# Optimization experiments

Measured on AMD Instinct MI355X. Metric: run time of the kernel, lower is better.

The kernel has to match this reference:

```python
import jax, jax.numpy as jnp
import numpy as np


def setup_inputs() -> dict:
    key = jax.random.key(0)
    k1, k2, k3 = jax.random.split(key, 3)
    B, N, D = 4, 4096, 1024
    x = jax.random.normal(k1, (B, N, D), dtype=jnp.float32)
    # torch nn.Linear default init ~ U(-1/sqrt(D), 1/sqrt(D)); scale normals similarly
    scale = 1.0 / np.sqrt(D)
    Wq = jax.random.normal(k2, (D, D), dtype=jnp.float32) * scale
    Wk = jax.random.normal(k3, (D, D), dtype=jnp.float32) * scale
    return {"x": x, "Wq": Wq, "Wk": Wk}


def reference(x, Wq, Wk):
    # torch Linear: y = x @ W.T (weight shape [out, in])
    D = x.shape[-1]
    q = jnp.einsum('bnd,ed->bne', x, Wq)  # [B,N,D]
    k = jnp.einsum('bnd,ed->bne', x, Wk)  # [B,N,D]
    scores = jnp.einsum('bqd,bkd->bqk', q, k) / jnp.sqrt(jnp.float32(D))
    attn = jax.nn.softmax(scores, axis=-1)  # [B,N,N]
    return jnp.einsum('bqk,bkd->bqd', attn, x)
```

## Files before the change

### kernel.cpp

```cpp
#include <hip/hip_runtime.h>
#include <stdint.h>
#include <math.h>

typedef __attribute__((ext_vector_type(8))) short short8;
typedef __attribute__((ext_vector_type(4))) float fx4;
typedef unsigned int u32;

#define MFMA16(a, b, c) __builtin_amdgcn_mfma_f32_16x16x32_bf16(a, b, c, 0, 0, 0)
#define SCL 0.04508422002777948f

#define CFENCE asm volatile("" ::: "memory")

__device__ __forceinline__ unsigned short f2bfu(float f) {
  unsigned u = __builtin_bit_cast(unsigned, f);
  u += 0x7fffu + ((u >> 16) & 1u);
  return (unsigned short)(u >> 16);
}

__device__ __forceinline__ float fast_exp2(float x) {
  float r;
  asm("v_exp_f32 %0, %1" : "=v"(r) : "v"(x));
  return r;
}

__device__ __forceinline__ void gl_lds16(const void* g, void* l) {
  __builtin_amdgcn_global_load_lds(
      (const __attribute__((address_space(1))) u32*)g,
      (__attribute__((address_space(3))) u32*)l, 16, 0, 0);
}

__device__ __forceinline__ void barx() {
  CFENCE;
  __builtin_amdgcn_s_barrier();
  CFENCE;
}

__global__ __launch_bounds__(256) void prep_kernel(const float* __restrict__ x,
                                                   unsigned short* __restrict__ xT,
                                                   unsigned short* __restrict__ xbf) {
  __shared__ float tile[64 * 65];
  const int b = blockIdx.z, n0 = blockIdx.x * 64, d0 = blockIdx.y * 64;
  const int tid = threadIdx.x;
  const float* xb = x + ((size_t)b * 4096 + n0) * 1024 + d0;
#pragma unroll
  for (int i = 0; i < 4; i++) {
    int idx = tid + 256 * i;
    int r = idx >> 4, c4 = (idx & 15) * 4;
    const float4 v = *(const float4*)(xb + (size_t)r * 1024 + c4);
    float* tp = &tile[r * 65 + c4];
    tp[0] = v.x; tp[1] = v.y; tp[2] = v.z; tp[3] = v.w;
    uint2 pkt;
    pkt.x = (u32)f2bfu(v.x) | ((u32)f2bfu(v.y) << 16);
    pkt.y = (u32)f2bfu(v.z) | ((u32)f2bfu(v.w) << 16);
    *(uint2*)(xbf + ((size_t)b * 4096 + n0 + r) * 1024 + d0 + c4) = pkt;
  }
  __syncthreads();
  unsigned short* xo = xT + ((size_t)b * 1024 + d0) * 4096 + n0;
#pragma unroll
  for (int i = 0; i < 4; i++) {
    int idx = tid + 256 * i;
    int dr = idx >> 4, n4 = (idx & 15) * 4;
    unsigned short h0 = f2bfu(tile[(n4 + 0) * 65 + dr]);
    unsigned short h1 = f2bfu(tile[(n4 + 1) * 65 + dr]);
    unsigned short h2 = f2bfu(tile[(n4 + 2) * 65 + dr]);
    unsigned short h3 = f2bfu(tile[(n4 + 3) * 65 + dr]);
    uint2 pkt;
    pkt.x = (u32)h0 | ((u32)h1 << 16);
    pkt.y = (u32)h2 | ((u32)h3 << 16);
    *(uint2*)(xo + (size_t)dr * 4096 + n4) = pkt;
  }
}

__global__ __launch_bounds__(256) void wconv_kernel(const float* __restrict__ Wq,
                                                    const float* __restrict__ Wk,
                                                    unsigned short* __restrict__ Wqb,
                                                    unsigned short* __restrict__ Wkb) {
  int gid = blockIdx.x * 256 + threadIdx.x;
  const float* s = (gid < 262144) ? Wq : Wk;
  unsigned short* d = (gid < 262144) ? Wqb : Wkb;
  int off = (gid & 262143) * 4;
  const float4 v = *(const float4*)(s + off);
  uint2 pkt;
  pkt.x = (u32)f2bfu(v.x) | ((u32)f2bfu(v.y) << 16);
  pkt.y = (u32)f2bfu(v.z) | ((u32)f2bfu(v.w) << 16);
  *(uint2*)(d + off) = pkt;
}


template <int ONES, int NT, int LDA, int LDB>
__device__ __forceinline__ void core128(const unsigned short* __restrict__ Ab,
                                        const unsigned short* __restrict__ Bb,
                                        short* lds, fx4 (&acc)[4][4], fx4 (&accl)[4]) {
  constexpr int BUFB = 49152;
  const int tid = threadIdx.x;
  const int wave = tid >> 6, lane = tid & 63;
  const int wm = wave >> 1, wn = wave & 1;
  const int quad = lane >> 4, l16 = lane & 15;
  char* lp = (char*)lds;

  const int sr0 = tid >> 3, so0 = (tid & 7) ^ (sr0 & 7);
  const int ga0 = sr0 * LDA + so0 * 8;
  const int ga1 = ga0 + 64 * LDA;
  const int gb0 = sr0 * LDB + so0 * 8;
  const int ld0 = tid * 16;

  const int cst0 = (quad ^ (l16 & 7)) * 16;
  const int cst1 = ((4 + quad) ^ (l16 & 7)) * 16;
  const int arb = (wm >> 1) * 16384 + (wm & 1) * 8192 + l16 * 128;
  const int brb = 32768 + wn * 8192 + l16 * 128;

  short8 ones;
#pragma unroll
  for (int i = 0; i < 8; i++) ones[i] = (short)0x3F80;
#pragma unroll
  for (int i = 0; i < 4; i++) {
    accl[i] = (fx4)0.f;
#pragma unroll
    for (int j = 0; j < 4; j++) acc[i][j] = (fx4)0.f;
  }

#define PV_STGA(halfb, rowadd, bufb, kte)                                          \
  do {                                                                             \
    gl_lds16(Ab + (size_t)(rowadd) * LDA + (kte) + ga0, lp + (bufb) + (halfb) + ld0); \
    gl_lds16(Ab + (size_t)(rowadd) * LDA + (kte) + ga1,                            \
             lp + (bufb) + (halfb) + ld0 + 8192);                                  \
  } while (0)
#define PV_STGB(halfb, rowadd, bufb, kte) \
  gl_lds16(Bb + (size_t)(rowadd) * LDB + (kte) + gb0, lp + (bufb) + 32768 + (halfb) + ld0)

  PV_STGB(0, 0, 0, 0);
  PV_STGA(0, 0, 0, 0);
  PV_STGA(16384, 128, 0, 0);
  PV_STGB(8192, 64, 0, 0);
  PV_STGB(0, 0, BUFB, 64);
  PV_STGA(0, 0, BUFB, 64);
  asm volatile("s_waitcnt vmcnt(3)" ::: "memory");
  barx();

  short8 af[4], bf0[4], bf1[4];
  for (int t = 0; t < NT; ++t) {
    const int cbo = (t & 1) * BUFB, nbo = cbo ^ BUFB;
    const int kt1 = ((t + 1) & (NT - 1)) * 64;
    const int kt2 = ((t + 2) & (NT - 1)) * 64;
#pragma unroll
    for (int mt = 0; mt < 2; mt++) {
      af[2 * mt] = *(const short8*)(lp + cbo + arb + mt * 2048 + cst0);
      af[2 * mt + 1] = *(const short8*)(lp + cbo + arb + mt * 2048 + cst1);
    }
#pragma unroll
    for (int nt = 0; nt < 2; nt++) {
      bf0[2 * nt] = *(const short8*)(lp + cbo + brb + nt * 2048 + cst0);
      bf0[2 * nt + 1] = *(const short8*)(lp + cbo + brb + nt * 2048 + cst1);
    }
    PV_STGA(16384, 128, nbo, kt1);
    barx();
    __builtin_amdgcn_s_setprio(1);
#pragma unroll
    for (int mt = 0; mt < 2; mt++) {
#pragma unroll
      for (int nt = 0; nt < 2; nt++) {
        acc[mt][nt] = MFMA16(af[2 * mt], bf0[2 * nt], acc[mt][nt]);
        acc[mt][nt] = MFMA16(af[2 * mt + 1], bf0[2 * nt + 1], acc[mt][nt]);
      }
      if (ONES) {
        accl[mt] = MFMA16(af[2 * mt], ones, accl[mt]);
        accl[mt] = MFMA16(af[2 * mt + 1], ones, accl[mt]);
      }
    }
    __builtin_amdgcn_s_setprio(0);
    barx();
#pragma unroll
    for (int nt = 0; nt < 2; nt++) {
      bf1[2 * nt] = *(const short8*)(lp + cbo + brb + (nt + 2) * 2048 + cst0);
      bf1[2 * nt + 1] = *(const short8*)(lp + cbo + brb + (nt + 2) * 2048 + cst1);
    }
    PV_STGB(8192, 64, nbo, kt1);
    barx();
    __builtin_amdgcn_s_setprio(1);
#pragma unroll
    for (int mt = 0; mt < 2; mt++)
#pragma unroll
      for (int nt = 0; nt < 2; nt++) {
        acc[mt][nt + 2] = MFMA16(af[2 * mt], bf1[2 * nt], acc[mt][nt + 2]);
        acc[mt][nt + 2] = MFMA16(af[2 * mt + 1], bf1[2 * nt + 1], acc[mt][nt + 2]);
      }
    __builtin_amdgcn_s_setprio(0);
    barx();
#pragma unroll
    for (int mt = 0; mt < 2; mt++) {
      af[2 * mt] = *(const short8*)(lp + cbo + arb + (mt + 2) * 2048 + cst0);
      af[2 * mt + 1] = *(const short8*)(lp + cbo + arb + (mt + 2) * 2048 + cst1);
    }
    PV_STGB(0, 0, cbo, kt2);
    barx();
    __builtin_amdgcn_s_setprio(1);
#pragma unroll
    for (int mt = 0; mt < 2; mt++) {
#pragma unroll
      for (int nt = 0; nt < 2; nt++) {
        acc[mt + 2][nt + 2] = MFMA16(af[2 * mt], bf1[2 * nt], acc[mt + 2][nt + 2]);
        acc[mt + 2][nt + 2] = MFMA16(af[2 * mt + 1], bf1[2 * nt + 1], acc[mt + 2][nt + 2]);
      }
      if (ONES) {
        accl[mt + 2] = MFMA16(af[2 * mt], ones, accl[mt + 2]);
        accl[mt + 2] = MFMA16(af[2 * mt + 1], ones, accl[mt + 2]);
      }
    }
    __builtin_amdgcn_s_setprio(0);
    barx();
    PV_STGA(0, 0, cbo, kt2);
    asm volatile("s_waitcnt vmcnt(3)" ::: "memory");
    barx();
    __builtin_amdgcn_s_setprio(1);
#pragma unroll
    for (int mt = 0; mt < 2; mt++)
#pragma unroll
      for (int nt = 0; nt < 2; nt++) {
        acc[mt + 2][nt] = MFMA16(af[2 * mt], bf0[2 * nt], acc[mt + 2][nt]);
        acc[mt + 2][nt] = MFMA16(af[2 * mt + 1], bf0[2 * nt + 1], acc[mt + 2][nt]);
      }
    __builtin_amdgcn_s_setprio(0);
    barx();
  }
#undef PV_STGA
#undef PV_STGB
}

__global__ __launch_bounds__(512) void proj_kernel(
    const unsigned short* __restrict__ xbf, const unsigned short* __restrict__ Wqb,
    const unsigned short* __restrict__ Wkb, unsigned short* __restrict__ Qo,
    unsigned short* __restrict__ Ko) {
  __shared__ __attribute__((aligned(16))) short lds[49152];
  const unsigned short* Wb = blockIdx.z ? Wkb : Wqb;
  unsigned short* O = blockIdx.z ? Ko : Qo;
  const int m0 = blockIdx.x * 256, e0 = blockIdx.y * 128;
  fx4 acc[4][4], accl[4];
  core128<0, 16, 1024, 1024>(xbf + (size_t)m0 * 1024, Wb + (size_t)e0 * 1024, lds, acc, accl);
  const int wave = threadIdx.x >> 6, lane = threadIdx.x & 63;
  const int wm = wave >> 1, wn = wave & 1;
  const int quad = lane >> 4, l16 = lane & 15;
#pragma unroll
  for (int mt = 0; mt < 4; mt++) {
    const int row = m0 + wm * 64 + mt * 16 + quad * 4;
#pragma unroll
    for (int nt = 0; nt < 4; nt++) {
      const int col = e0 + wn * 64 + nt * 16 + l16;
      unsigned short* op = O + (size_t)row * 1024 + col;
#pragma unroll
      for (int i = 0; i < 4; i++) op[(size_t)i * 1024] = f2bfu(acc[mt][nt][i]);
    }
  }
}

__global__ __launch_bounds__(512) void pv_kernel(
    const unsigned short* __restrict__ P, const unsigned short* __restrict__ xT,
    unsigned short* __restrict__ Ost, int bbase) {
  __shared__ __attribute__((aligned(16))) short lds[49152];
  const int bz = blockIdx.z, b = bbase + bz;
  const int m0 = blockIdx.x * 256, e0 = blockIdx.y * 128;
  const unsigned short* Ab = P + (size_t)bz * 4096 * 4096 + (size_t)m0 * 4096;
  const unsigned short* Bb = xT + (size_t)b * 1024 * 4096 + (size_t)e0 * 4096;
  fx4 acc[4][4], accl[4];
  core128<1, 64, 4096, 4096>(Ab, Bb, lds, acc, accl);
  unsigned short* O = Ost + (size_t)b * 4096 * 1024;
  const int wave = threadIdx.x >> 6, lane = threadIdx.x & 63;
  const int wm = wave >> 1, wn = wave & 1;
  const int quad = lane >> 4, l16 = lane & 15;
#pragma unroll
  for (int mt = 0; mt < 4; mt++) {
    const int row = m0 + wm * 64 + mt * 16 + quad * 4;
    const fx4 li = accl[mt];
    fx4 r;
#pragma unroll
    for (int i = 0; i < 4; i++) r[i] = __builtin_amdgcn_rcpf(li[i]);
#pragma unroll
    for (int nt = 0; nt < 4; nt++) {
      const int col = e0 + wn * 64 + nt * 16 + l16;
      unsigned short* op = O + (size_t)row * 1024 + col;
#pragma unroll
      for (int i = 0; i < 4; i++) op[(size_t)i * 1024] = f2bfu(acc[mt][nt][i] * r[i]);
    }
  }
}

__global__ __launch_bounds__(512) void qk_kernel(
    const unsigned short* __restrict__ Qb, const unsigned short* __restrict__ Kb,
    unsigned short* __restrict__ Pp, int bbase) {
  constexpr int NT = 16;
  __shared__ __attribute__((aligned(16))) short lds[65536];
  const int bz = blockIdx.z, b = bbase + bz;
  const unsigned short* A = Qb + (size_t)b * 4096 * 1024;
  const unsigned short* Bm = Kb + (size_t)b * 4096 * 1024;
  unsigned short* Pb = Pp + (size_t)bz * 4096 * 4096;
  const int m0 = blockIdx.x * 256, n0 = blockIdx.y * 256;
  const int tid = threadIdx.x;
  const int wave = tid >> 6, lane = tid & 63;
  const int wm = wave >> 2, wn = wave & 3;
  const int quad = lane >> 4, l16 = lane & 15;
  char* lp = (char*)lds;

  const unsigned short* Ab = A + (size_t)m0 * 1024;
  const unsigned short* Bb = Bm + (size_t)n0 * 1024;
  const int sr0 = tid >> 3, so0 = (tid & 7) ^ (sr0 & 7);
  const int ga0 = sr0 * 1024 + so0 * 8;
  const int ga1 = ga0 + 64 * 1024;
  const int ld0 = tid * 16;

  const int cst0 = (quad ^ (l16 & 7)) * 16;
  const int cst1 = ((4 + quad) ^ (l16 & 7)) * 16;
  const int arb = wm * 16384 + l16 * 128;
  const int brb = 32768 + (wn >> 1) * 16384 + (wn & 1) * 8192 + l16 * 128;

  fx4 acc[8][4];
#pragma unroll
  for (int i = 0; i < 8; i++)
#pragma unroll
    for (int j = 0; j < 4; j++) acc[i][j] = (fx4)0.f;

#define QK_STG(OPb, halfb, rowadd, bufb, kte)                                       \
  do {                                                                              \
    gl_lds16(OPb + (size_t)(rowadd) * 1024 + (kte) + ga0, lp + (bufb) + (halfb) + ld0); \
    gl_lds16(OPb + (size_t)(rowadd) * 1024 + (kte) + ga1,                           \
             lp + (bufb) + (halfb) + ld0 + 8192);                                   \
  } while (0)

  QK_STG(Bb, 32768, 0, 0, 0);
  QK_STG(Ab, 0, 0, 0, 0);
  QK_STG(Ab, 16384, 128, 0, 0);
  QK_STG(Bb, 49152, 128, 0, 0);
  QK_STG(Bb, 32768, 0, 65536, 64);
  QK_STG(Ab, 0, 0, 65536, 64);
  asm volatile("s_waitcnt vmcnt(4)" ::: "memory");
  barx();

  short8 af[8], bf0[4], bf1[4];
  for (int t = 0; t < NT; ++t) {
    const int cbo = (t & 1) * 65536, nbo = cbo ^ 65536;
    const int kt1 = ((t + 1) & (NT - 1)) * 64;
    const int kt2 = ((t + 2) & (NT - 1)) * 64;
#pragma unroll
    for (int mt = 0; mt < 4; mt++) {
      af[2 * mt] = *(const short8*)(lp + cbo + arb + mt * 2048 + cst0);
      af[2 * mt + 1] = *(const short8*)(lp + cbo + arb + mt * 2048 + cst1);
    }
#pragma unroll
    for (int nt = 0; nt < 2; nt++) {
      bf0[2 * nt] = *(const short8*)(lp + cbo + brb + nt * 2048 + cst0);
      bf0[2 * nt + 1] = *(const short8*)(lp + cbo + brb + nt * 2048 + cst1);
    }
    QK_STG(Ab, 16384, 128, nbo, kt1);
    barx();
    __builtin_amdgcn_s_setprio(1);
#pragma unroll
    for (int mt = 0; mt < 4; mt++)
#pragma unroll
      for (int nt = 0; nt < 2; nt++) {
        acc[mt][nt] = MFMA16(af[2 * mt], bf0[2 * nt], acc[mt][nt]);
        acc[mt][nt] = MFMA16(af[2 * mt + 1], bf0[2 * nt + 1], acc[mt][nt]);
      }
    __builtin_amdgcn_s_setprio(0);
    barx();
#pragma unroll
    for (int nt = 0; nt < 2; nt++) {
      bf1[2 * nt] = *(const short8*)(lp + cbo + brb + (nt + 2) * 2048 + cst0);
      bf1[2 * nt + 1] = *(const short8*)(lp + cbo + brb + (nt + 2) * 2048 + cst1);
    }
    QK_STG(Bb, 49152, 128, nbo, kt1);
    barx();
    __builtin_amdgcn_s_setprio(1);
#pragma unroll
    for (int mt = 0; mt < 4; mt++)
#pragma unroll
      for (int nt = 0; nt < 2; nt++) {
        acc[mt][nt + 2] = MFMA16(af[2 * mt], bf1[2 * nt], acc[mt][nt + 2]);
        acc[mt][nt + 2] = MFMA16(af[2 * mt + 1], bf1[2 * nt + 1], acc[mt][nt + 2]);
      }
    __builtin_amdgcn_s_setprio(0);
    barx();
#pragma unroll
    for (int mt = 0; mt < 4; mt++) {
      af[2 * mt] = *(const short8*)(lp + cbo + arb + (mt + 4) * 2048 + cst0);
      af[2 * mt + 1] = *(const short8*)(lp + cbo + arb + (mt + 4) * 2048 + cst1);
    }
    QK_STG(Bb, 32768, 0, cbo, kt2);
    barx();
    __builtin_amdgcn_s_setprio(1);
#pragma unroll
    for (int mt = 0; mt < 4; mt++)
#pragma unroll
      for (int nt = 0; nt < 2; nt++) {
        acc[mt + 4][nt + 2] = MFMA16(af[2 * mt], bf1[2 * nt], acc[mt + 4][nt + 2]);
        acc[mt + 4][nt + 2] = MFMA16(af[2 * mt + 1], bf1[2 * nt + 1], acc[mt + 4][nt + 2]);
      }
    __builtin_amdgcn_s_setprio(0);
    barx();
    QK_STG(Ab, 0, 0, cbo, kt2);
    asm volatile("s_waitcnt vmcnt(4)" ::: "memory");
    barx();
    __builtin_amdgcn_s_setprio(1);
#pragma unroll
    for (int mt = 0; mt < 4; mt++)
#pragma unroll
      for (int nt = 0; nt < 2; nt++) {
        acc[mt + 4][nt] = MFMA16(af[2 * mt], bf0[2 * nt], acc[mt + 4][nt]);
        acc[mt + 4][nt] = MFMA16(af[2 * mt + 1], bf0[2 * nt + 1], acc[mt + 4][nt]);
      }
    __builtin_amdgcn_s_setprio(0);
    barx();
  }
#undef QK_STG
#pragma unroll
  for (int mt = 0; mt < 8; mt++) {
    const int row = m0 + wm * 128 + mt * 16 + quad * 4;
#pragma unroll
    for (int nt = 0; nt < 4; nt++) {
      const int col = n0 + wn * 64 + nt * 16 + l16;
      unsigned short* pp = Pb + (size_t)row * 4096 + col;
#pragma unroll
      for (int i = 0; i < 4; i++)
        pp[(size_t)i * 4096] = f2bfu(fast_exp2(acc[mt][nt][i] * SCL));
    }
  }
}

__global__ __launch_bounds__(256) void fin_kernel(const uint4* __restrict__ Ost,
                                                  float4* __restrict__ out) {
  size_t t = (size_t)blockIdx.x * 256 + threadIdx.x;
  const uint4 v = Ost[t];
  float4 o0, o1;
  o0.x = __builtin_bit_cast(float, v.x << 16);
  o0.y = __builtin_bit_cast(float, v.x & 0xffff0000u);
  o0.z = __builtin_bit_cast(float, v.y << 16);
  o0.w = __builtin_bit_cast(float, v.y & 0xffff0000u);
  o1.x = __builtin_bit_cast(float, v.z << 16);
  o1.y = __builtin_bit_cast(float, v.z & 0xffff0000u);
  o1.z = __builtin_bit_cast(float, v.w << 16);
  o1.w = __builtin_bit_cast(float, v.w & 0xffff0000u);
  out[t * 2] = o0;
  out[t * 2 + 1] = o1;
}

extern "C" void kernel_launch(void* const* d_in, const int* in_sizes, int n_in,
                              void* d_out, int out_size, void* d_ws, size_t ws_size,
                              hipStream_t stream) {
  const float* x = (const float*)d_in[0];
  const float* Wq = (const float*)d_in[1];
  const float* Wk = (const float*)d_in[2];
  char* ws = (char*)d_ws;
  unsigned short* xT = (unsigned short*)ws;
  unsigned short* Qb = (unsigned short*)(ws + (size_t)33554432);
  unsigned short* Kb = (unsigned short*)(ws + (size_t)67108864);
  unsigned short* Ost = Qb;
  unsigned short* xbf = (unsigned short*)d_out;
  unsigned short* Wqb = (unsigned short*)((char*)d_out + (size_t)33554432);
  unsigned short* Wkb = (unsigned short*)((char*)d_out + (size_t)35651584);
  unsigned short* Pp = (unsigned short*)d_out;

  hipLaunchKernelGGL(prep_kernel, dim3(64, 16, 4), dim3(256), 0, stream, x, xT, xbf);
  hipLaunchKernelGGL(wconv_kernel, dim3(2048), dim3(256), 0, stream, Wq, Wk, Wqb, Wkb);
  hipLaunchKernelGGL(proj_kernel, dim3(64, 8, 2), dim3(512), 0, stream, xbf, Wqb, Wkb, Qb, Kb);
  hipLaunchKernelGGL(qk_kernel, dim3(16, 16, 2), dim3(512), 0, stream, Qb, Kb, Pp, 0);
  hipLaunchKernelGGL(pv_kernel, dim3(16, 8, 2), dim3(512), 0, stream, Pp, xT, Ost, 0);
  hipLaunchKernelGGL(qk_kernel, dim3(16, 16, 2), dim3(512), 0, stream, Qb, Kb, Pp, 2);
  hipLaunchKernelGGL(pv_kernel, dim3(16, 8, 2), dim3(512), 0, stream, Pp, xT, Ost, 2);
  hipLaunchKernelGGL(fin_kernel, dim3(8192), dim3(256), 0, stream,
                     (const uint4*)Ost, (float4*)d_out);
}
```

Measured before the change: 497.1 us.

## Share 256x256 GEMM core for projection and swizzle block order in QK/PV

```diff
diff --git a/kernel.cpp b/kernel.cpp
--- a/kernel.cpp
+++ b/kernel.cpp
@@ -86,6 +86,123 @@
   *(uint2*)(d + off) = pkt;
 }
 
+__device__ __forceinline__ void core256(const unsigned short* __restrict__ Ab,
+                                        const unsigned short* __restrict__ Bb,
+                                        char* lp, fx4 (&acc)[8][4]) {
+  constexpr int NT = 16;
+  const int tid = threadIdx.x;
+  const int wave = tid >> 6, lane = tid & 63;
+  const int wm = wave >> 2, wn = wave & 3;
+  const int quad = lane >> 4, l16 = lane & 15;
+
+  const int sr0 = tid >> 3, so0 = (tid & 7) ^ (sr0 & 7);
+  const int ga0 = sr0 * 1024 + so0 * 8;
+  const int ga1 = ga0 + 64 * 1024;
+  const int ld0 = tid * 16;
+
+  const int cst0 = (quad ^ (l16 & 7)) * 16;
+  const int cst1 = ((4 + quad) ^ (l16 & 7)) * 16;
+  const int arb = wm * 16384 + l16 * 128;
+  const int brb = 32768 + (wn >> 1) * 16384 + (wn & 1) * 8192 + l16 * 128;
+
+#pragma unroll
+  for (int i = 0; i < 8; i++)
+#pragma unroll
+    for (int j = 0; j < 4; j++) acc[i][j] = (fx4)0.f;
+
+#define C_STG(OPb, halfb, rowadd, bufb, kte)                                        \
+  do {                                                                              \
+    gl_lds16(OPb + (size_t)(rowadd) * 1024 + (kte) + ga0, lp + (bufb) + (halfb) + ld0); \
+    gl_lds16(OPb + (size_t)(rowadd) * 1024 + (kte) + ga1,                           \
+             lp + (bufb) + (halfb) + ld0 + 8192);                                   \
+  } while (0)
+
+  C_STG(Bb, 32768, 0, 0, 0);
+  C_STG(Ab, 0, 0, 0, 0);
+  C_STG(Ab, 16384, 128, 0, 0);
+  C_STG(Bb, 49152, 128, 0, 0);
+  C_STG(Bb, 32768, 0, 65536, 64);
+  C_STG(Ab, 0, 0, 65536, 64);
+  asm volatile("s_waitcnt vmcnt(4)" ::: "memory");
+  barx();
+
+  short8 af[8], bf0[4], bf1[4];
+  for (int t = 0; t < NT; ++t) {
+    const int cbo = (t & 1) * 65536, nbo = cbo ^ 65536;
+    const int kt1 = ((t + 1) & (NT - 1)) * 64;
+    const int kt2 = ((t + 2) & (NT - 1)) * 64;
+#pragma unroll
+    for (int mt = 0; mt < 4; mt++) {
+      af[2 * mt] = *(const short8*)(lp + cbo + arb + mt * 2048 + cst0);
+      af[2 * mt + 1] = *(const short8*)(lp + cbo + arb + mt * 2048 + cst1);
+    }
+#pragma unroll
+    for (int nt = 0; nt < 2; nt++) {
+      bf0[2 * nt] = *(const short8*)(lp + cbo + brb + nt * 2048 + cst0);
+      bf0[2 * nt + 1] = *(const short8*)(lp + cbo + brb + nt * 2048 + cst1);
+    }
+    C_STG(Ab, 16384, 128, nbo, kt1);
+    barx();
+    __builtin_amdgcn_s_setprio(1);
+#pragma unroll
+    for (int mt = 0; mt < 4; mt++)
+#pragma unroll
+      for (int nt = 0; nt < 2; nt++) {
+        acc[mt][nt] = MFMA16(af[2 * mt], bf0[2 * nt], acc[mt][nt]);
+        acc[mt][nt] = MFMA16(af[2 * mt + 1], bf0[2 * nt + 1], acc[mt][nt]);
+      }
+    __builtin_amdgcn_s_setprio(0);
+    barx();
+#pragma unroll
+    for (int nt = 0; nt < 2; nt++) {
+      bf1[2 * nt] = *(const short8*)(lp + cbo + brb + (nt + 2) * 2048 + cst0);
+      bf1[2 * nt + 1] = *(const short8*)(lp + cbo + brb + (nt + 2) * 2048 + cst1);
+    }
+    C_STG(Bb, 49152, 128, nbo, kt1);
+    barx();
+    __builtin_amdgcn_s_setprio(1);
+#pragma unroll
+    for (int mt = 0; mt < 4; mt++)
+#pragma unroll
+      for (int nt = 0; nt < 2; nt++) {
+        acc[mt][nt + 2] = MFMA16(af[2 * mt], bf1[2 * nt], acc[mt][nt + 2]);
+        acc[mt][nt + 2] = MFMA16(af[2 * mt + 1], bf1[2 * nt + 1], acc[mt][nt + 2]);
+      }
+    __builtin_amdgcn_s_setprio(0);
+    barx();
+#pragma unroll
+    for (int mt = 0; mt < 4; mt++) {
+      af[2 * mt] = *(const short8*)(lp + cbo + arb + (mt + 4) * 2048 + cst0);
+      af[2 * mt + 1] = *(const short8*)(lp + cbo + arb + (mt + 4) * 2048 + cst1);
+    }
+    C_STG(Bb, 32768, 0, cbo, kt2);
+    barx();
+    __builtin_amdgcn_s_setprio(1);
+#pragma unroll
+    for (int mt = 0; mt < 4; mt++)
+#pragma unroll
+      for (int nt = 0; nt < 2; nt++) {
+        acc[mt + 4][nt + 2] = MFMA16(af[2 * mt], bf1[2 * nt], acc[mt + 4][nt + 2]);
+        acc[mt + 4][nt + 2] = MFMA16(af[2 * mt + 1], bf1[2 * nt + 1], acc[mt + 4][nt + 2]);
+      }
+    __builtin_amdgcn_s_setprio(0);
+    barx();
+    C_STG(Ab, 0, 0, cbo, kt2);
+    asm volatile("s_waitcnt vmcnt(4)" ::: "memory");
+    barx();
+    __builtin_amdgcn_s_setprio(1);
+#pragma unroll
+    for (int mt = 0; mt < 4; mt++)
+#pragma unroll
+      for (int nt = 0; nt < 2; nt++) {
+        acc[mt + 4][nt] = MFMA16(af[2 * mt], bf0[2 * nt], acc[mt + 4][nt]);
+        acc[mt + 4][nt] = MFMA16(af[2 * mt + 1], bf0[2 * nt + 1], acc[mt + 4][nt]);
+      }
+    __builtin_amdgcn_s_setprio(0);
+    barx();
+  }
+#undef C_STG
+}
 
 template <int ONES, int NT, int LDA, int LDB>
 __device__ __forceinline__ void core128(const unsigned short* __restrict__ Ab,
@@ -230,24 +347,54 @@
     const unsigned short* __restrict__ xbf, const unsigned short* __restrict__ Wqb,
     const unsigned short* __restrict__ Wkb, unsigned short* __restrict__ Qo,
     unsigned short* __restrict__ Ko) {
-  __shared__ __attribute__((aligned(16))) short lds[49152];
+  __shared__ __attribute__((aligned(16))) short lds[65536];
   const unsigned short* Wb = blockIdx.z ? Wkb : Wqb;
   unsigned short* O = blockIdx.z ? Ko : Qo;
-  const int m0 = blockIdx.x * 256, e0 = blockIdx.y * 128;
-  fx4 acc[4][4], accl[4];
-  core128<0, 16, 1024, 1024>(xbf + (size_t)m0 * 1024, Wb + (size_t)e0 * 1024, lds, acc, accl);
+  const int m0 = blockIdx.x * 256, e0 = blockIdx.y * 256;
+  fx4 acc[8][4];
+  core256(xbf + (size_t)m0 * 1024, Wb + (size_t)e0 * 1024, (char*)lds, acc);
   const int wave = threadIdx.x >> 6, lane = threadIdx.x & 63;
-  const int wm = wave >> 1, wn = wave & 1;
+  const int wm = wave >> 2, wn = wave & 3;
   const int quad = lane >> 4, l16 = lane & 15;
 #pragma unroll
-  for (int mt = 0; mt < 4; mt++) {
-    const int row = m0 + wm * 64 + mt * 16 + quad * 4;
+  for (int mt = 0; mt < 8; mt++) {
+    const int row = m0 + wm * 128 + mt * 16 + quad * 4;
 #pragma unroll
     for (int nt = 0; nt < 4; nt++) {
       const int col = e0 + wn * 64 + nt * 16 + l16;
       unsigned short* op = O + (size_t)row * 1024 + col;
 #pragma unroll
       for (int i = 0; i < 4; i++) op[(size_t)i * 1024] = f2bfu(acc[mt][nt][i]);
+    }
+  }
+}
+
+__global__ __launch_bounds__(512) void qk_kernel(
+    const unsigned short* __restrict__ Qb, const unsigned short* __restrict__ Kb,
+    unsigned short* __restrict__ Pp, int bbase) {
+  __shared__ __attribute__((aligned(16))) short lds[65536];
+  const int fid = blockIdx.x + 16 * blockIdx.y + 256 * blockIdx.z;
+  const int swz = (fid & 7) * 64 + (fid >> 3);
+  const int bx = swz & 15, by = (swz >> 4) & 15, bz = swz >> 8;
+  const int b = bbase + bz;
+  unsigned short* Pb = Pp + (size_t)bz * 4096 * 4096;
+  const int m0 = bx * 256, n0 = by * 256;
+  fx4 acc[8][4];
+  core256(Qb + (size_t)b * 4096 * 1024 + (size_t)m0 * 1024,
+          Kb + (size_t)b * 4096 * 1024 + (size_t)n0 * 1024, (char*)lds, acc);
+  const int wave = threadIdx.x >> 6, lane = threadIdx.x & 63;
+  const int wm = wave >> 2, wn = wave & 3;
+  const int quad = lane >> 4, l16 = lane & 15;
+#pragma unroll
+  for (int mt = 0; mt < 8; mt++) {
+    const int row = m0 + wm * 128 + mt * 16 + quad * 4;
+#pragma unroll
+    for (int nt = 0; nt < 4; nt++) {
+      const int col = n0 + wn * 64 + nt * 16 + l16;
+      unsigned short* pp = Pb + (size_t)row * 4096 + col;
+#pragma unroll
+      for (int i = 0; i < 4; i++)
+        pp[(size_t)i * 4096] = f2bfu(fast_exp2(acc[mt][nt][i] * SCL));
     }
   }
 }
@@ -256,8 +403,11 @@
     const unsigned short* __restrict__ P, const unsigned short* __restrict__ xT,
     unsigned short* __restrict__ Ost, int bbase) {
   __shared__ __attribute__((aligned(16))) short lds[49152];
-  const int bz = blockIdx.z, b = bbase + bz;
-  const int m0 = blockIdx.x * 256, e0 = blockIdx.y * 128;
+  const int fid = blockIdx.x + 16 * blockIdx.y + 128 * blockIdx.z;
+  const int swz = (fid & 7) * 32 + (fid >> 3);
+  const int bx = swz & 15, by = (swz >> 4) & 7, bz = swz >> 7;
+  const int b = bbase + bz;
+  const int m0 = bx * 256, e0 = by * 128;
   const unsigned short* Ab = P + (size_t)bz * 4096 * 4096 + (size_t)m0 * 4096;
   const unsigned short* Bb = xT + (size_t)b * 1024 * 4096 + (size_t)e0 * 4096;
   fx4 acc[4][4], accl[4];
@@ -279,146 +429,6 @@
       unsigned short* op = O + (size_t)row * 1024 + col;
 #pragma unroll
       for (int i = 0; i < 4; i++) op[(size_t)i * 1024] = f2bfu(acc[mt][nt][i] * r[i]);
-    }
-  }
-}
-
-__global__ __launch_bounds__(512) void qk_kernel(
-    const unsigned short* __restrict__ Qb, const unsigned short* __restrict__ Kb,
-    unsigned short* __restrict__ Pp, int bbase) {
-  constexpr int NT = 16;
-  __shared__ __attribute__((aligned(16))) short lds[65536];
-  const int bz = blockIdx.z, b = bbase + bz;
-  const unsigned short* A = Qb + (size_t)b * 4096 * 1024;
-  const unsigned short* Bm = Kb + (size_t)b * 4096 * 1024;
-  unsigned short* Pb = Pp + (size_t)bz * 4096 * 4096;
-  const int m0 = blockIdx.x * 256, n0 = blockIdx.y * 256;
-  const int tid = threadIdx.x;
-  const int wave = tid >> 6, lane = tid & 63;
-  const int wm = wave >> 2, wn = wave & 3;
-  const int quad = lane >> 4, l16 = lane & 15;
-  char* lp = (char*)lds;
-
-  const unsigned short* Ab = A + (size_t)m0 * 1024;
-  const unsigned short* Bb = Bm + (size_t)n0 * 1024;
-  const int sr0 = tid >> 3, so0 = (tid & 7) ^ (sr0 & 7);
-  const int ga0 = sr0 * 1024 + so0 * 8;
-  const int ga1 = ga0 + 64 * 1024;
-  const int ld0 = tid * 16;
-
-  const int cst0 = (quad ^ (l16 & 7)) * 16;
-  const int cst1 = ((4 + quad) ^ (l16 & 7)) * 16;
-  const int arb = wm * 16384 + l16 * 128;
-  const int brb = 32768 + (wn >> 1) * 16384 + (wn & 1) * 8192 + l16 * 128;
-
-  fx4 acc[8][4];
-#pragma unroll
-  for (int i = 0; i < 8; i++)
-#pragma unroll
-    for (int j = 0; j < 4; j++) acc[i][j] = (fx4)0.f;
-
-#define QK_STG(OPb, halfb, rowadd, bufb, kte)                                       \
-  do {                                                                              \
-    gl_lds16(OPb + (size_t)(rowadd) * 1024 + (kte) + ga0, lp + (bufb) + (halfb) + ld0); \
-    gl_lds16(OPb + (size_t)(rowadd) * 1024 + (kte) + ga1,                           \
-             lp + (bufb) + (halfb) + ld0 + 8192);                                   \
-  } while (0)
-
-  QK_STG(Bb, 32768, 0, 0, 0);
-  QK_STG(Ab, 0, 0, 0, 0);
-  QK_STG(Ab, 16384, 128, 0, 0);
-  QK_STG(Bb, 49152, 128, 0, 0);
-  QK_STG(Bb, 32768, 0, 65536, 64);
-  QK_STG(Ab, 0, 0, 65536, 64);
-  asm volatile("s_waitcnt vmcnt(4)" ::: "memory");
-  barx();
-
-  short8 af[8], bf0[4], bf1[4];
-  for (int t = 0; t < NT; ++t) {
-    const int cbo = (t & 1) * 65536, nbo = cbo ^ 65536;
-    const int kt1 = ((t + 1) & (NT - 1)) * 64;
-    const int kt2 = ((t + 2) & (NT - 1)) * 64;
-#pragma unroll
-    for (int mt = 0; mt < 4; mt++) {
-      af[2 * mt] = *(const short8*)(lp + cbo + arb + mt * 2048 + cst0);
-      af[2 * mt + 1] = *(const short8*)(lp + cbo + arb + mt * 2048 + cst1);
-    }
-#pragma unroll
-    for (int nt = 0; nt < 2; nt++) {
-      bf0[2 * nt] = *(const short8*)(lp + cbo + brb + nt * 2048 + cst0);
-      bf0[2 * nt + 1] = *(const short8*)(lp + cbo + brb + nt * 2048 + cst1);
-    }
-    QK_STG(Ab, 16384, 128, nbo, kt1);
-    barx();
-    __builtin_amdgcn_s_setprio(1);
-#pragma unroll
-    for (int mt = 0; mt < 4; mt++)
-#pragma unroll
-      for (int nt = 0; nt < 2; nt++) {
-        acc[mt][nt] = MFMA16(af[2 * mt], bf0[2 * nt], acc[mt][nt]);
-        acc[mt][nt] = MFMA16(af[2 * mt + 1], bf0[2 * nt + 1], acc[mt][nt]);
-      }
-    __builtin_amdgcn_s_setprio(0);
-    barx();
-#pragma unroll
-    for (int nt = 0; nt < 2; nt++) {
-      bf1[2 * nt] = *(const short8*)(lp + cbo + brb + (nt + 2) * 2048 + cst0);
-      bf1[2 * nt + 1] = *(const short8*)(lp + cbo + brb + (nt + 2) * 2048 + cst1);
-    }
-    QK_STG(Bb, 49152, 128, nbo, kt1);
-    barx();
-    __builtin_amdgcn_s_setprio(1);
-#pragma unroll
-    for (int mt = 0; mt < 4; mt++)
-#pragma unroll
-      for (int nt = 0; nt < 2; nt++) {
-        acc[mt][nt + 2] = MFMA16(af[2 * mt], bf1[2 * nt], acc[mt][nt + 2]);
-        acc[mt][nt + 2] = MFMA16(af[2 * mt + 1], bf1[2 * nt + 1], acc[mt][nt + 2]);
-      }
-    __builtin_amdgcn_s_setprio(0);
-    barx();
-#pragma unroll
-    for (int mt = 0; mt < 4; mt++) {
-      af[2 * mt] = *(const short8*)(lp + cbo + arb + (mt + 4) * 2048 + cst0);
-      af[2 * mt + 1] = *(const short8*)(lp + cbo + arb + (mt + 4) * 2048 + cst1);
-    }
-    QK_STG(Bb, 32768, 0, cbo, kt2);
-    barx();
-    __builtin_amdgcn_s_setprio(1);
-#pragma unroll
-    for (int mt = 0; mt < 4; mt++)
-#pragma unroll
-      for (int nt = 0; nt < 2; nt++) {
-        acc[mt + 4][nt + 2] = MFMA16(af[2 * mt], bf1[2 * nt], acc[mt + 4][nt + 2]);
-        acc[mt + 4][nt + 2] = MFMA16(af[2 * mt + 1], bf1[2 * nt + 1], acc[mt + 4][nt + 2]);
-      }
-    __builtin_amdgcn_s_setprio(0);
-    barx();
-    QK_STG(Ab, 0, 0, cbo, kt2);
-    asm volatile("s_waitcnt vmcnt(4)" ::: "memory");
-    barx();
-    __builtin_amdgcn_s_setprio(1);
-#pragma unroll
-    for (int mt = 0; mt < 4; mt++)
-#pragma unroll
-      for (int nt = 0; nt < 2; nt++) {
-        acc[mt + 4][nt] = MFMA16(af[2 * mt], bf0[2 * nt], acc[mt + 4][nt]);
-        acc[mt + 4][nt] = MFMA16(af[2 * mt + 1], bf0[2 * nt + 1], acc[mt + 4][nt]);
-      }
-    __builtin_amdgcn_s_setprio(0);
-    barx();
-  }
-#undef QK_STG
-#pragma unroll
-  for (int mt = 0; mt < 8; mt++) {
-    const int row = m0 + wm * 128 + mt * 16 + quad * 4;
-#pragma unroll
-    for (int nt = 0; nt < 4; nt++) {
-      const int col = n0 + wn * 64 + nt * 16 + l16;
-      unsigned short* pp = Pb + (size_t)row * 4096 + col;
-#pragma unroll
-      for (int i = 0; i < 4; i++)
-        pp[(size_t)i * 4096] = f2bfu(fast_exp2(acc[mt][nt][i] * SCL));
     }
   }
 }
@@ -458,7 +468,7 @@
 
   hipLaunchKernelGGL(prep_kernel, dim3(64, 16, 4), dim3(256), 0, stream, x, xT, xbf);
   hipLaunchKernelGGL(wconv_kernel, dim3(2048), dim3(256), 0, stream, Wq, Wk, Wqb, Wkb);
-  hipLaunchKernelGGL(proj_kernel, dim3(64, 8, 2), dim3(512), 0, stream, xbf, Wqb, Wkb, Qb, Kb);
+  hipLaunchKernelGGL(proj_kernel, dim3(64, 4, 2), dim3(512), 0, stream, xbf, Wqb, Wkb, Qb, Kb);
   hipLaunchKernelGGL(qk_kernel, dim3(16, 16, 2), dim3(512), 0, stream, Qb, Kb, Pp, 0);
   hipLaunchKernelGGL(pv_kernel, dim3(16, 8, 2), dim3(512), 0, stream, Pp, xT, Ost, 0);
   hipLaunchKernelGGL(qk_kernel, dim3(16, 16, 2), dim3(512), 0, stream, Qb, Kb, Pp, 2);
```

Result: faster. 468.6 us (-5.7%).
